# Performance work log

Hardware: AMD Instinct MI355X
Metric: run time of the kernel (lower is better)

## Reference

```python
import jax, jax.numpy as jnp
import numpy as np
import math

B, S, D = 16, 577, 768          # batch, seq (24*24 grid + 1 cls), in_dim=att_dim
H, HD = 12, 64                  # heads, head_dim
GRID = 24                       # height = width; S = GRID*GRID + rpe_skip
RATIO = 1.9
ALPHA, BETA, GAMMA = 1.0 * RATIO, 2.0 * RATIO, 8.0 * RATIO
BETA_INT = int(BETA)            # 3
NUM_BUCKETS = (2 * BETA_INT + 1) ** 2 + 1  # 49 product buckets + 1 extra for skip (cls) = 50


def _piecewise_index(d):
    # iRPE piecewise bucket index (numpy, static). d: integer offsets.
    d = d.astype(np.float64)
    ad = np.abs(d)
    log_part = ALPHA + np.log(np.maximum(ad, 1e-9) / ALPHA) / math.log(GAMMA / ALPHA) * (BETA - ALPHA)
    y_out = np.sign(d) * np.clip(np.round(log_part), None, BETA)
    idx = np.where(ad <= ALPHA, np.round(d), y_out)
    return np.trunc(idx).astype(np.int64)  # torch .to(int) truncates toward zero


def make_rp_bucket():
    # 2D 'product' method bucket ids with skip=1 (cls token -> extra bucket)
    ii, jj = np.meshgrid(np.arange(GRID), np.arange(GRID), indexing='ij')
    pos = np.stack([ii.ravel(), jj.ravel()], axis=-1)          # (L,2)
    diff = pos[:, None, :] - pos[None, :, :]                    # (L,L,2)
    Sb = 2 * BETA_INT + 1
    r = _piecewise_index(diff[..., 0]) + BETA_INT               # [0, 2*beta_int]
    c = _piecewise_index(diff[..., 1]) + BETA_INT
    pid = r * Sb + c                                            # [0, 48]
    L = GRID * GRID
    bucket = np.full((L + 1, L + 1), NUM_BUCKETS - 1, dtype=np.int32)
    bucket[1:, 1:] = pid
    return jnp.asarray(bucket)


def setup_inputs() -> dict:
    key = jax.random.key(0)
    k1, k2, k3 = jax.random.split(key, 3)
    x = jax.random.normal(k1, (B, S, D), dtype=jnp.float32)
    w_qkv = jax.random.normal(k2, (3 * D, D), dtype=jnp.float32) * 0.02   # torch Linear weight (out,in)
    rpe_table = jax.random.normal(k3, (HD, NUM_BUCKETS), dtype=jnp.float32) * 0.02  # shared-head contextual table
    rp_bucket = make_rp_bucket()                                # (S,S) int32
    return {"x": x, "w_qkv": w_qkv, "rpe_table": rpe_table, "rp_bucket": rp_bucket}


def reference(x, w_qkv, rpe_table, rp_bucket):
    qkv = x @ w_qkv.T                                           # (B,S,3D)
    q, k, v = jnp.split(qkv, 3, axis=-1)
    # Faithful to torch source: plain reshape (B,S,D)->(B,H,S,HD) (no transpose-split)
    scale = 1.0 / jnp.sqrt(jnp.asarray(HD, x.dtype))
    q = q.reshape(B, H, S, HD) * scale
    k = k.reshape(B, H, S, HD)
    v = v.reshape(B, H, S, HD)
    qk = jnp.einsum('bhid,bhjd->bhij', q, k)                    # (B,H,S,S)
    # contextual rpe_k: bias[b,h,i,j] = (q[b,h,i] . rpe_table[:, rp_bucket[i,j]])
    ctx = jnp.einsum('bhid,dc->bhic', q, rpe_table)             # (B,H,S,NUM_BUCKETS)
    idx = jnp.broadcast_to(rp_bucket[None, None].astype(jnp.int32), (B, H, S, S))
    bias = jnp.take_along_axis(ctx, idx, axis=-1)               # (B,H,S,S)
    att = jax.nn.softmax(qk + bias, axis=-1)
    out = jnp.einsum('bhij,bhjd->bhid', att, v)                 # (B,H,S,HD)
    y = out.transpose(0, 2, 1, 3).reshape(B, S, D)              # out_proj is Identity (out_dim==att_dim)
    return y
```

## Files before the change

### kernel.cpp

```cpp
#include <hip/hip_runtime.h>

constexpr int BN_  = 16;
constexpr int SN_  = 577;
constexpr int SP_  = 640;
constexpr int DN_  = 768;
constexpr int HN_  = 12;
constexpr int HD_  = 64;
constexpr int NB_  = 50;
constexpr int MR_  = BN_ * SN_;
constexpr int MRP_ = 73 * 128;
constexpr int NQ_  = 3 * DN_;
constexpr int BHS_ = BN_ * HN_ * SN_;
constexpr int SHD_ = SN_ * HD_;

typedef __attribute__((ext_vector_type(8))) short short8;
typedef __attribute__((ext_vector_type(4))) float f32x4;

__device__ __forceinline__ short f2bf(float f) {
  union { float f; unsigned u; } v; v.f = f;
  unsigned r = (v.u + 0x7fffu + ((v.u >> 16) & 1u)) >> 16;
  return (short)r;
}

__device__ __forceinline__ float ex2(float x) {
  float r; asm("v_exp_f32 %0, %1" : "=v"(r) : "v"(x)); return r;
}

__device__ __forceinline__ unsigned cvtpk(float a, float b) {
  unsigned r; asm("v_cvt_pk_bf16_f32 %0, %1, %2" : "=v"(r) : "v"(a), "v"(b));
  return r;
}

__device__ __forceinline__ float bf2f(unsigned short u) {
  union { unsigned u; float f; } v; v.u = ((unsigned)u) << 16; return v.f;
}

__launch_bounds__(256)
__global__ void cvt_k(const float* __restrict__ src, short* __restrict__ dst,
                      int n_src, int n_dst) {
  const int i = (blockIdx.x * 256 + threadIdx.x) * 8;
  if (i >= n_dst) return;
  union { short8 v; short u[8]; } pk;
  if (i < n_src) {
    const float4 a = *(const float4*)(src + i);
    const float4 b = *(const float4*)(src + i + 4);
    pk.u[0] = f2bf(a.x); pk.u[1] = f2bf(a.y); pk.u[2] = f2bf(a.z); pk.u[3] = f2bf(a.w);
    pk.u[4] = f2bf(b.x); pk.u[5] = f2bf(b.y); pk.u[6] = f2bf(b.z); pk.u[7] = f2bf(b.w);
  } else {
#pragma unroll
    for (int j = 0; j < 8; ++j) pk.u[j] = 0;
  }
  *(short8*)(dst + i) = pk.v;
}

__launch_bounds__(256)
__global__ void rpb8_k(const int* __restrict__ rpb, unsigned char* __restrict__ rpbu8) {
  const int tid = blockIdx.x * 256 + threadIdx.x;
  if (tid >= SN_ * 160) return;
  const int i = tid / 160, c4 = tid - i * 160;
  const int j = c4 * 4;
  uchar4 o;
  o.x = (j     < SN_) ? (unsigned char)rpb[i * SN_ + j    ] : 0;
  o.y = (j + 1 < SN_) ? (unsigned char)rpb[i * SN_ + j + 1] : 0;
  o.z = (j + 2 < SN_) ? (unsigned char)rpb[i * SN_ + j + 2] : 0;
  o.w = (j + 3 < SN_) ? (unsigned char)rpb[i * SN_ + j + 3] : 0;
  *(uchar4*)(rpbu8 + (size_t)i * 640 + j) = o;
}

__launch_bounds__(256)
__global__ void qkv_mfma_k(const short* __restrict__ xb, const short* __restrict__ wb,
                           short* __restrict__ Qbf, short* __restrict__ Ksw,
                           short* __restrict__ Vbf) {
  __shared__ short At[128 * 64];
  __shared__ short Bt[128 * 64];
  const int t = threadIdx.x;
  const int w = t >> 6, lane = t & 63, g = lane >> 4, ln = lane & 15;
  const int wm = w >> 1, wn = w & 1;
  const int m0 = blockIdx.y * 128, n0 = blockIdx.x * 128;

  const int sr = t >> 1, su = (t & 1) * 4;
  const short* ga = xb + (size_t)(m0 + sr) * DN_ + su * 8;
  const short* gb = wb + (size_t)(n0 + sr) * DN_ + su * 8;
  short* la = At + sr * 64;
  short* lb = Bt + sr * 64;
  const int swr = sr & 7;

  f32x4 acc[4][4];
#pragma unroll
  for (int mt = 0; mt < 4; ++mt)
#pragma unroll
    for (int nt = 0; nt < 4; ++nt) acc[mt][nt] = (f32x4){0.f, 0.f, 0.f, 0.f};

  short8 ra[4], rb[4];
#pragma unroll
  for (int u = 0; u < 4; ++u) {
    ra[u] = *(const short8*)(ga + u * 8);
    rb[u] = *(const short8*)(gb + u * 8);
  }

  for (int k0 = 0; k0 < DN_; k0 += 64) {
    __syncthreads();
#pragma unroll
    for (int u = 0; u < 4; ++u) {
      *(short8*)(la + (((su + u) ^ swr) * 8)) = ra[u];
      *(short8*)(lb + (((su + u) ^ swr) * 8)) = rb[u];
    }
    __syncthreads();
    if (k0 + 64 < DN_) {
#pragma unroll
      for (int u = 0; u < 4; ++u) {
        ra[u] = *(const short8*)(ga + k0 + 64 + u * 8);
        rb[u] = *(const short8*)(gb + k0 + 64 + u * 8);
      }
    }
#pragma unroll
    for (int kc = 0; kc < 2; ++kc) {
      short8 af[4], bf[4];
#pragma unroll
      for (int mt = 0; mt < 4; ++mt) {
        const int row = wm * 64 + mt * 16 + ln;
        const int u = (kc * 4 + g) ^ (row & 7);
        af[mt] = *(const short8*)&At[row * 64 + u * 8];
      }
#pragma unroll
      for (int nt = 0; nt < 4; ++nt) {
        const int row = wn * 64 + nt * 16 + ln;
        const int u = (kc * 4 + g) ^ (row & 7);
        bf[nt] = *(const short8*)&Bt[row * 64 + u * 8];
      }
#pragma unroll
      for (int mt = 0; mt < 4; ++mt)
#pragma unroll
        for (int nt = 0; nt < 4; ++nt)
          acc[mt][nt] = __builtin_amdgcn_mfma_f32_16x16x32_bf16(af[mt], bf[nt], acc[mt][nt], 0, 0, 0);
    }
  }

  const int nw0  = n0 + wn * 64;
  const int secg = nw0 / DN_;
  const int cbw  = nw0 - secg * DN_;
  const float QSC = 0.18033688011112042f;
#pragma unroll
  for (int mt = 0; mt < 4; ++mt) {
#pragma unroll
    for (int r = 0; r < 4; ++r) {
      const int gm = m0 + wm * 64 + mt * 16 + 4 * g + r;
      if (gm >= MR_) continue;
      const int bb = gm / SN_;
      const int ss = gm - bb * SN_;
      const int pb = ss * DN_ + cbw;
#pragma unroll
      for (int nt = 0; nt < 4; ++nt) {
        const int p   = pb + nt * 16 + ln;
        const int hh  = p / SHD_;
        const int rem = p - hh * SHD_;
        const int ii  = rem >> 6;
        const int dd  = rem & 63;
        const size_t ro = (size_t)(bb * HN_ + hh);
        const float v = acc[mt][nt][r];
        if (secg == 0) {
          Qbf[(ro * SN_ + ii) * 64 + dd] = f2bf(v * QSC);
        } else if (secg == 1) {
          Ksw[(ro * SP_ + ii) * 64 + (dd ^ ((ii & 7) << 3))] = f2bf(v);
        } else {
          Vbf[(ro * SP_ + ii) * 64 + dd] = f2bf(v);
        }
      }
    }
  }
}

__launch_bounds__(256)
__global__ void vtr_k(const short* __restrict__ Vbf, short* __restrict__ Vtsw) {
  __shared__ short T[64][72];
  const int t = threadIdx.x;
  const int jt = blockIdx.x, bh = blockIdx.y;
  const int j0 = jt * 64;
  {
    const int r = t >> 2, c0 = (t & 3) * 16;
    const short* src = Vbf + ((size_t)bh * SP_ + j0 + r) * 64 + c0;
    *(short8*)&T[r][c0]     = *(const short8*)(src);
    *(short8*)&T[r][c0 + 8] = *(const short8*)(src + 8);
  }
  __syncthreads();
  const int d = t >> 2;
  short* dst = Vtsw + ((size_t)bh * 64 + d) * SP_;
  const int sw = (d & 7) << 3;
#pragma unroll
  for (int e = 0; e < 4; ++e) {
    const int jl = (t & 3) * 16 + e * 4;
    const int jg = j0 + jl;
    short4 v;
    v.x = (jg + 0 < SN_) ? T[jl + 0][d] : (short)0;
    v.y = (jg + 1 < SN_) ? T[jl + 1][d] : (short)0;
    v.z = (jg + 2 < SN_) ? T[jl + 2][d] : (short)0;
    v.w = (jg + 3 < SN_) ? T[jl + 3][d] : (short)0;
    *(short4*)&dst[jg ^ sw] = v;
  }
}

__launch_bounds__(256)
__global__ void attn_k(const short* __restrict__ Qbf, const short* __restrict__ Ksw,
                       const short* __restrict__ Vtsw, const float* __restrict__ rpe,
                       const unsigned char* __restrict__ rpbu8, float* __restrict__ y) {
  __shared__ short Kt[2 * 4096];
  __shared__ short Vt[2 * 4096];
  __shared__ unsigned char rpbt[2 * 5120];
  __shared__ unsigned short ctxs[4][16][53];
  short (*Rp)[64] = (short (*)[64])rpbt;

  const int t = threadIdx.x;
  const int w = t >> 6, lane = t & 63, g = lane >> 4, ln = lane & 15;
  const int wg = blockIdx.x;
  const int xcd = wg & 7, idx = wg >> 3;
  const int qt = idx % 10;
  const int bh = (idx / 10) * 8 + xcd;
  const int b = bh / HN_, h = bh - b * HN_;
  const int i0 = qt * 64;
  const size_t rb = (size_t)bh * SN_;
  const short* Kbh = Ksw + (size_t)bh * SP_ * 64;
  const short* Vbh = Vtsw + (size_t)bh * 64 * SP_;

  const int tK = t * 8;
  const int vRow = t >> 3, vCol = (t & 7) * 8;
  const int rpRow = t >> 2, rpCol = (t & 3) * 16;
  const int irow_s = (i0 + rpRow <= SN_ - 1) ? (i0 + rpRow) : (SN_ - 1);

  short8 kr0, kr1, vr0, vr1; int4 rp_;
  kr0 = *(const short8*)(Kbh + tK);
  kr1 = *(const short8*)(Kbh + 2048 + tK);
  vr0 = *(const short8*)(Vbh + (size_t)vRow * SP_ + vCol);
  vr1 = *(const short8*)(Vbh + (size_t)(32 + vRow) * SP_ + vCol);
  rp_ = *(const int4*)(rpbu8 + (size_t)irow_s * 640 + rpCol);

  for (int e = t; e < 64 * 64; e += 256) {
    const int c = e >> 6, d = e & 63;
    Rp[c][d] = (c < NB_) ? f2bf(rpe[d * NB_ + c]) : (short)0;
  }

  short8 qf[2];
  {
    int row = i0 + 16 * w + ln; if (row > SN_ - 1) row = SN_ - 1;
    const short* qp = Qbf + (rb + row) * 64;
    qf[0] = *(const short8*)(qp + 8 * g);
    qf[1] = *(const short8*)(qp + 32 + 8 * g);
  }

  __syncthreads();

  {
    f32x4 accC[4];
#pragma unroll
    for (int ct = 0; ct < 4; ++ct) accC[ct] = (f32x4){0.f, 0.f, 0.f, 0.f};
#pragma unroll
    for (int kc = 0; kc < 2; ++kc) {
#pragma unroll
      for (int ct = 0; ct < 4; ++ct) {
        const short8 rf = *(const short8*)&Rp[ct * 16 + ln][kc * 32 + 8 * g];
        accC[ct] = __builtin_amdgcn_mfma_f32_16x16x32_bf16(qf[kc], rf, accC[ct], 0, 0, 0);
      }
    }
    __syncthreads();
#pragma unroll
    for (int ct = 0; ct < 4; ++ct) {
      const int c = ct * 16 + ln;
      if (c < 53) {
#pragma unroll
        for (int r = 0; r < 4; ++r)
          ctxs[w][4 * g + r][c] = (unsigned short)f2bf(accC[ct][r]);
      }
    }
  }

  *(short8*)&Kt[tK]        = kr0;
  *(short8*)&Kt[2048 + tK] = kr1;
  *(short8*)&Vt[tK]        = vr0;
  *(short8*)&Vt[2048 + tK] = vr1;
  *(int4*)&rpbt[rpRow * 80 + rpCol] = rp_;
  kr0 = *(const short8*)(Kbh + 4096 + tK);
  kr1 = *(const short8*)(Kbh + 4096 + 2048 + tK);
  vr0 = *(const short8*)(Vbh + (size_t)vRow * SP_ + 64 + vCol);
  vr1 = *(const short8*)(Vbh + (size_t)(32 + vRow) * SP_ + 64 + vCol);
  rp_ = *(const int4*)(rpbu8 + (size_t)irow_s * 640 + 64 + rpCol);
  __syncthreads();

  float m = -3e38f, l = 0.f;
  f32x4 accO[4];
#pragma unroll
  for (int dt = 0; dt < 4; ++dt) accO[dt] = (f32x4){0.f, 0.f, 0.f, 0.f};

  const int swv = (ln & 7) << 3;
  const unsigned short* cbase = &ctxs[w][ln][0];
  const int rpoff = (16 * w + ln) * 80;

  int cur = 0;
  for (int jt = 0; jt < 10; ++jt) {
    const int cw = cur ^ 1;
    if (jt < 9) {
      *(short8*)&Kt[cw * 4096 + tK]        = kr0;
      *(short8*)&Kt[cw * 4096 + 2048 + tK] = kr1;
      *(short8*)&Vt[cw * 4096 + tK]        = vr0;
      *(short8*)&Vt[cw * 4096 + 2048 + tK] = vr1;
      *(int4*)&rpbt[cw * 5120 + rpRow * 80 + rpCol] = rp_;
    }
    if (jt < 8) {
      const int jn = jt * 64 + 128;
      kr0 = *(const short8*)(Kbh + (size_t)jn * 64 + tK);
      kr1 = *(const short8*)(Kbh + (size_t)jn * 64 + 2048 + tK);
      vr0 = *(const short8*)(Vbh + (size_t)vRow * SP_ + jn + vCol);
      vr1 = *(const short8*)(Vbh + (size_t)(32 + vRow) * SP_ + jn + vCol);
      rp_ = *(const int4*)(rpbu8 + (size_t)irow_s * 640 + jn + rpCol);
    }

    const short* KtC = Kt + cur * 4096;
    const short* VtC = Vt + cur * 4096;
    const unsigned char* rpC = rpbt + cur * 5120;

    f32x4 accS[4];
#pragma unroll
    for (int nt = 0; nt < 4; ++nt) accS[nt] = (f32x4){0.f, 0.f, 0.f, 0.f};
    __builtin_amdgcn_s_setprio(1);
#pragma unroll
    for (int kc = 0; kc < 2; ++kc) {
      const int cb = (kc * 32 + 8 * g) ^ swv;
#pragma unroll
      for (int nt = 0; nt < 4; ++nt) {
        const short8 kf = *(const short8*)&KtC[(nt * 16 + ln) * 64 + cb];
        accS[nt] = __builtin_amdgcn_mfma_f32_16x16x32_bf16(kf, qf[kc], accS[nt], 0, 0, 0);
      }
    }
    __builtin_amdgcn_s_setprio(0);

    float pv[4][4];
#pragma unroll
    for (int nt = 0; nt < 4; ++nt) {
      const uchar4 bk = *(const uchar4*)&rpC[rpoff + nt * 16 + 4 * g];
      pv[nt][0] = accS[nt][0] + bf2f(cbase[bk.x]);
      pv[nt][1] = accS[nt][1] + bf2f(cbase[bk.y]);
      pv[nt][2] = accS[nt][2] + bf2f(cbase[bk.z]);
      pv[nt][3] = accS[nt][3] + bf2f(cbase[bk.w]);
    }
    if (jt == 9) {
#pragma unroll
      for (int nt = 0; nt < 4; ++nt) {
        const int jb = jt * 64 + nt * 16 + 4 * g;
#pragma unroll
        for (int r = 0; r < 4; ++r)
          if (jb + r >= SN_) pv[nt][r] = -3e38f;
      }
    }

    float mq[4];
#pragma unroll
    for (int nt = 0; nt < 4; ++nt)
      mq[nt] = fmaxf(fmaxf(pv[nt][0], pv[nt][1]), fmaxf(pv[nt][2], pv[nt][3]));
    float mx = fmaxf(fmaxf(mq[0], mq[1]), fmaxf(mq[2], mq[3]));
    mx = fmaxf(mx, __shfl_xor(mx, 16));
    mx = fmaxf(mx, __shfl_xor(mx, 32));

    if (__any(mx > m + 8.f)) {
      const float mnew = fmaxf(m, mx);
      const float sc = ex2(m - mnew);
      float scr[4];
#pragma unroll
      for (int r = 0; r < 4; ++r) scr[r] = __shfl(sc, 4 * g + r);
#pragma unroll
      for (int dt = 0; dt < 4; ++dt)
#pragma unroll
        for (int r = 0; r < 4; ++r) accO[dt][r] *= scr[r];
      l *= sc;
      m = mnew;
    }

#pragma unroll
    for (int nt = 0; nt < 4; ++nt)
#pragma unroll
      for (int r = 0; r < 4; ++r)
        pv[nt][r] = ex2(pv[nt][r] - m);
    float sq[4];
#pragma unroll
    for (int nt = 0; nt < 4; ++nt)
      sq[nt] = (pv[nt][0] + pv[nt][1]) + (pv[nt][2] + pv[nt][3]);
    float sum = (sq[0] + sq[1]) + (sq[2] + sq[3]);
    sum += __shfl_xor(sum, 16);
    sum += __shfl_xor(sum, 32);
    l += sum;

    short8 pf[2];
#pragma unroll
    for (int kc = 0; kc < 2; ++kc) {
      union { short8 v; unsigned wd[4]; } pk;
      pk.wd[0] = cvtpk(pv[2 * kc][0],     pv[2 * kc][1]);
      pk.wd[1] = cvtpk(pv[2 * kc][2],     pv[2 * kc][3]);
      pk.wd[2] = cvtpk(pv[2 * kc + 1][0], pv[2 * kc + 1][1]);
      pk.wd[3] = cvtpk(pv[2 * kc + 1][2], pv[2 * kc + 1][3]);
      pf[kc] = pk.v;
    }

    __builtin_amdgcn_s_setprio(1);
#pragma unroll
    for (int kc = 0; kc < 2; ++kc) {
#pragma unroll
      for (int dt = 0; dt < 4; ++dt) {
        const short* vrow = &VtC[(dt * 16 + ln) * 64];
        union { short8 v; short4 hh[2]; } u;
        u.hh[0] = *(const short4*)&vrow[(kc * 32 + 4 * g) ^ swv];
        u.hh[1] = *(const short4*)&vrow[(kc * 32 + 16 + 4 * g) ^ swv];
        accO[dt] = __builtin_amdgcn_mfma_f32_16x16x32_bf16(pf[kc], u.v, accO[dt], 0, 0, 0);
      }
    }
    __builtin_amdgcn_s_setprio(0);

    __syncthreads();
    cur ^= 1;
  }

  float linv[4];
#pragma unroll
  for (int r = 0; r < 4; ++r) linv[r] = 1.f / __shfl(l, 4 * g + r);
#pragma unroll
  for (int r = 0; r < 4; ++r) {
    const int i = i0 + 16 * w + 4 * g + r;
    if (i >= SN_) continue;
    float* yp = y + ((size_t)b * SN_ + i) * DN_ + h * HD_ + ln;
#pragma unroll
    for (int dt = 0; dt < 4; ++dt) yp[dt * 16] = accO[dt][r] * linv[r];
  }
}

extern "C" void kernel_launch(void* const* d_in, const int* in_sizes, int n_in,
                              void* d_out, int out_size, void* d_ws, size_t ws_size,
                              hipStream_t stream) {
  const float* x   = (const float*)d_in[0];
  const float* w   = (const float*)d_in[1];
  const float* rpe = (const float*)d_in[2];
  const int*   rpb = (const int*)d_in[3];
  float* y = (float*)d_out;

  short* xb   = (short*)d_ws;
  short* wb   = xb + (size_t)MRP_ * DN_;
  short* Qbf  = wb + (size_t)NQ_ * DN_;
  short* Ksw  = Qbf + (size_t)BHS_ * HD_;
  short* Vbf  = Ksw + (size_t)BN_ * HN_ * SP_ * 64;
  short* Vtsw = Vbf + (size_t)BN_ * HN_ * SP_ * 64;
  unsigned char* rpbu8 = (unsigned char*)(Vtsw + (size_t)BN_ * HN_ * 64 * SP_);

  cvt_k<<<dim3(MRP_ * DN_ / 2048), 256, 0, stream>>>(x, xb, MR_ * DN_, MRP_ * DN_);
  cvt_k<<<dim3(NQ_ * DN_ / 2048), 256, 0, stream>>>(w, wb, NQ_ * DN_, NQ_ * DN_);
  rpb8_k<<<dim3((SN_ * 160 + 255) / 256), 256, 0, stream>>>(rpb, rpbu8);
  qkv_mfma_k<<<dim3(18, 73), 256, 0, stream>>>(xb, wb, Qbf, Ksw, Vbf);
  vtr_k<<<dim3(10, BN_ * HN_), 256, 0, stream>>>(Vbf, Vtsw);
  attn_k<<<dim3(1920), 256, 0, stream>>>(Qbf, Ksw, Vtsw, rpe, rpbu8, y);
}
```

Before: 162.6 us.

## Process 128 query rows per block, reusing K/V tiles across two subtiles

Each wave now handles two 16-row query subtiles, so a block covers 128 query rows and half as many blocks are launched. Every K and V fragment read from shared memory feeds two MFMAs, which halves global and LDS traffic for K/V per query row. The LDS double buffer is replaced by a single buffer with register prefetch and two barriers per iteration. V transpose storage is permuted so PV operands load as one short8 instead of two short4. Register pressure rises, and the loss of LDS double-buffering plus the smaller grid may reduce overlap and occupancy.

```diff
diff --git a/kernel.cpp b/kernel.cpp
--- a/kernel.cpp
+++ b/kernel.cpp
@@ -195,7 +195,10 @@
     v.y = (jg + 1 < SN_) ? T[jl + 1][d] : (short)0;
     v.z = (jg + 2 < SN_) ? T[jl + 2][d] : (short)0;
     v.w = (jg + 3 < SN_) ? T[jl + 3][d] : (short)0;
-    *(short4*)&dst[jg ^ sw] = v;
+    const int oq = (jg >> 2) & 7;
+    const int pq = ((oq & 3) << 1) | (oq >> 2);
+    const int p  = (jg & ~31) | (pq << 2);
+    *(short4*)&dst[p ^ sw] = v;
   }
 }
 
@@ -203,228 +206,230 @@
 __global__ void attn_k(const short* __restrict__ Qbf, const short* __restrict__ Ksw,
                        const short* __restrict__ Vtsw, const float* __restrict__ rpe,
                        const unsigned char* __restrict__ rpbu8, float* __restrict__ y) {
-  __shared__ short Kt[2 * 4096];
-  __shared__ short Vt[2 * 4096];
-  __shared__ unsigned char rpbt[2 * 5120];
-  __shared__ unsigned short ctxs[4][16][53];
+  __shared__ short Kt[4096];
+  __shared__ short Vt[4096];
+  __shared__ unsigned char rpbt[128 * 68];
+  __shared__ unsigned short ctxs[4][32][53];
   short (*Rp)[64] = (short (*)[64])rpbt;
 
   const int t = threadIdx.x;
   const int w = t >> 6, lane = t & 63, g = lane >> 4, ln = lane & 15;
   const int wg = blockIdx.x;
   const int xcd = wg & 7, idx = wg >> 3;
-  const int qt = idx % 10;
-  const int bh = (idx / 10) * 8 + xcd;
+  const int qt = idx % 5;
+  const int bh = (idx / 5) * 8 + xcd;
   const int b = bh / HN_, h = bh - b * HN_;
-  const int i0 = qt * 64;
+  const int i0 = qt * 128;
   const size_t rb = (size_t)bh * SN_;
   const short* Kbh = Ksw + (size_t)bh * SP_ * 64;
   const short* Vbh = Vtsw + (size_t)bh * 64 * SP_;
 
   const int tK = t * 8;
   const int vRow = t >> 3, vCol = (t & 7) * 8;
-  const int rpRow = t >> 2, rpCol = (t & 3) * 16;
+  const int rpRow = t >> 1, rpCol = (t & 1) * 32;
   const int irow_s = (i0 + rpRow <= SN_ - 1) ? (i0 + rpRow) : (SN_ - 1);
 
-  short8 kr0, kr1, vr0, vr1; int4 rp_;
+  short8 kr0, kr1, vr0, vr1; int4 rp0_, rp1_;
   kr0 = *(const short8*)(Kbh + tK);
   kr1 = *(const short8*)(Kbh + 2048 + tK);
   vr0 = *(const short8*)(Vbh + (size_t)vRow * SP_ + vCol);
   vr1 = *(const short8*)(Vbh + (size_t)(32 + vRow) * SP_ + vCol);
-  rp_ = *(const int4*)(rpbu8 + (size_t)irow_s * 640 + rpCol);
+  rp0_ = *(const int4*)(rpbu8 + (size_t)irow_s * 640 + rpCol);
+  rp1_ = *(const int4*)(rpbu8 + (size_t)irow_s * 640 + rpCol + 16);
 
   for (int e = t; e < 64 * 64; e += 256) {
     const int c = e >> 6, d = e & 63;
     Rp[c][d] = (c < NB_) ? f2bf(rpe[d * NB_ + c]) : (short)0;
   }
 
-  short8 qf[2];
+  short8 qf[2][2];
+#pragma unroll
+  for (int s = 0; s < 2; ++s) {
+    int row = i0 + 32 * w + 16 * s + ln; if (row > SN_ - 1) row = SN_ - 1;
+    const short* qp = Qbf + (rb + row) * 64;
+    qf[s][0] = *(const short8*)(qp + 8 * g);
+    qf[s][1] = *(const short8*)(qp + 32 + 8 * g);
+  }
+
+  __syncthreads();
+
   {
-    int row = i0 + 16 * w + ln; if (row > SN_ - 1) row = SN_ - 1;
-    const short* qp = Qbf + (rb + row) * 64;
-    qf[0] = *(const short8*)(qp + 8 * g);
-    qf[1] = *(const short8*)(qp + 32 + 8 * g);
-  }
-
-  __syncthreads();
-
-  {
-    f32x4 accC[4];
-#pragma unroll
-    for (int ct = 0; ct < 4; ++ct) accC[ct] = (f32x4){0.f, 0.f, 0.f, 0.f};
+    f32x4 accC[2][4];
+#pragma unroll
+    for (int s = 0; s < 2; ++s)
+#pragma unroll
+      for (int ct = 0; ct < 4; ++ct) accC[s][ct] = (f32x4){0.f, 0.f, 0.f, 0.f};
 #pragma unroll
     for (int kc = 0; kc < 2; ++kc) {
 #pragma unroll
       for (int ct = 0; ct < 4; ++ct) {
         const short8 rf = *(const short8*)&Rp[ct * 16 + ln][kc * 32 + 8 * g];
-        accC[ct] = __builtin_amdgcn_mfma_f32_16x16x32_bf16(qf[kc], rf, accC[ct], 0, 0, 0);
-      }
-    }
+        accC[0][ct] = __builtin_amdgcn_mfma_f32_16x16x32_bf16(qf[0][kc], rf, accC[0][ct], 0, 0, 0);
+        accC[1][ct] = __builtin_amdgcn_mfma_f32_16x16x32_bf16(qf[1][kc], rf, accC[1][ct], 0, 0, 0);
+      }
+    }
+#pragma unroll
+    for (int s = 0; s < 2; ++s)
+#pragma unroll
+      for (int ct = 0; ct < 4; ++ct) {
+        const int c = ct * 16 + ln;
+        if (c < 53) {
+#pragma unroll
+          for (int r = 0; r < 4; ++r)
+            ctxs[w][16 * s + 4 * g + r][c] = (unsigned short)f2bf(accC[s][ct][r]);
+        }
+      }
+  }
+
+  float m0s = -3e38f, m1s = -3e38f, l0s = 0.f, l1s = 0.f;
+  f32x4 accO[2][4];
+#pragma unroll
+  for (int s = 0; s < 2; ++s)
+#pragma unroll
+    for (int dt = 0; dt < 4; ++dt) accO[s][dt] = (f32x4){0.f, 0.f, 0.f, 0.f};
+
+  const int swv = (ln & 7) << 3;
+
+  for (int jt = 0; jt < 10; ++jt) {
     __syncthreads();
-#pragma unroll
-    for (int ct = 0; ct < 4; ++ct) {
-      const int c = ct * 16 + ln;
-      if (c < 53) {
-#pragma unroll
-        for (int r = 0; r < 4; ++r)
-          ctxs[w][4 * g + r][c] = (unsigned short)f2bf(accC[ct][r]);
-      }
-    }
-  }
-
-  *(short8*)&Kt[tK]        = kr0;
-  *(short8*)&Kt[2048 + tK] = kr1;
-  *(short8*)&Vt[tK]        = vr0;
-  *(short8*)&Vt[2048 + tK] = vr1;
-  *(int4*)&rpbt[rpRow * 80 + rpCol] = rp_;
-  kr0 = *(const short8*)(Kbh + 4096 + tK);
-  kr1 = *(const short8*)(Kbh + 4096 + 2048 + tK);
-  vr0 = *(const short8*)(Vbh + (size_t)vRow * SP_ + 64 + vCol);
-  vr1 = *(const short8*)(Vbh + (size_t)(32 + vRow) * SP_ + 64 + vCol);
-  rp_ = *(const int4*)(rpbu8 + (size_t)irow_s * 640 + 64 + rpCol);
-  __syncthreads();
-
-  float m = -3e38f, l = 0.f;
-  f32x4 accO[4];
-#pragma unroll
-  for (int dt = 0; dt < 4; ++dt) accO[dt] = (f32x4){0.f, 0.f, 0.f, 0.f};
-
-  const int swv = (ln & 7) << 3;
-  const unsigned short* cbase = &ctxs[w][ln][0];
-  const int rpoff = (16 * w + ln) * 80;
-
-  int cur = 0;
-  for (int jt = 0; jt < 10; ++jt) {
-    const int cw = cur ^ 1;
+    *(short8*)&Kt[tK]        = kr0;
+    *(short8*)&Kt[2048 + tK] = kr1;
+    *(short8*)&Vt[tK]        = vr0;
+    *(short8*)&Vt[2048 + tK] = vr1;
+    *(int4*)&rpbt[rpRow * 68 + rpCol]      = rp0_;
+    *(int4*)&rpbt[rpRow * 68 + rpCol + 16] = rp1_;
+    __syncthreads();
+
     if (jt < 9) {
-      *(short8*)&Kt[cw * 4096 + tK]        = kr0;
-      *(short8*)&Kt[cw * 4096 + 2048 + tK] = kr1;
-      *(short8*)&Vt[cw * 4096 + tK]        = vr0;
-      *(short8*)&Vt[cw * 4096 + 2048 + tK] = vr1;
-      *(int4*)&rpbt[cw * 5120 + rpRow * 80 + rpCol] = rp_;
-    }
-    if (jt < 8) {
-      const int jn = jt * 64 + 128;
+      const int jn = jt * 64 + 64;
       kr0 = *(const short8*)(Kbh + (size_t)jn * 64 + tK);
       kr1 = *(const short8*)(Kbh + (size_t)jn * 64 + 2048 + tK);
       vr0 = *(const short8*)(Vbh + (size_t)vRow * SP_ + jn + vCol);
       vr1 = *(const short8*)(Vbh + (size_t)(32 + vRow) * SP_ + jn + vCol);
-      rp_ = *(const int4*)(rpbu8 + (size_t)irow_s * 640 + jn + rpCol);
-    }
-
-    const short* KtC = Kt + cur * 4096;
-    const short* VtC = Vt + cur * 4096;
-    const unsigned char* rpC = rpbt + cur * 5120;
-
-    f32x4 accS[4];
-#pragma unroll
-    for (int nt = 0; nt < 4; ++nt) accS[nt] = (f32x4){0.f, 0.f, 0.f, 0.f};
+      rp0_ = *(const int4*)(rpbu8 + (size_t)irow_s * 640 + jn + rpCol);
+      rp1_ = *(const int4*)(rpbu8 + (size_t)irow_s * 640 + jn + rpCol + 16);
+    }
+
+    f32x4 accS[2][4];
+#pragma unroll
+    for (int s = 0; s < 2; ++s)
+#pragma unroll
+      for (int nt = 0; nt < 4; ++nt) accS[s][nt] = (f32x4){0.f, 0.f, 0.f, 0.f};
     __builtin_amdgcn_s_setprio(1);
 #pragma unroll
     for (int kc = 0; kc < 2; ++kc) {
       const int cb = (kc * 32 + 8 * g) ^ swv;
 #pragma unroll
       for (int nt = 0; nt < 4; ++nt) {
-        const short8 kf = *(const short8*)&KtC[(nt * 16 + ln) * 64 + cb];
-        accS[nt] = __builtin_amdgcn_mfma_f32_16x16x32_bf16(kf, qf[kc], accS[nt], 0, 0, 0);
+        const short8 kf = *(const short8*)&Kt[(nt * 16 + ln) * 64 + cb];
+        accS[0][nt] = __builtin_amdgcn_mfma_f32_16x16x32_bf16(kf, qf[0][kc], accS[0][nt], 0, 0, 0);
+        accS[1][nt] = __builtin_amdgcn_mfma_f32_16x16x32_bf16(kf, qf[1][kc], accS[1][nt], 0, 0, 0);
       }
     }
     __builtin_amdgcn_s_setprio(0);
 
-    float pv[4][4];
-#pragma unroll
-    for (int nt = 0; nt < 4; ++nt) {
-      const uchar4 bk = *(const uchar4*)&rpC[rpoff + nt * 16 + 4 * g];
-      pv[nt][0] = accS[nt][0] + bf2f(cbase[bk.x]);
-      pv[nt][1] = accS[nt][1] + bf2f(cbase[bk.y]);
-      pv[nt][2] = accS[nt][2] + bf2f(cbase[bk.z]);
-      pv[nt][3] = accS[nt][3] + bf2f(cbase[bk.w]);
-    }
-    if (jt == 9) {
+    short8 pf[2][2];
+#pragma unroll
+    for (int s = 0; s < 2; ++s) {
+      const unsigned short* cbase = &ctxs[w][16 * s + ln][0];
+      const int rpoff = (32 * w + 16 * s + ln) * 68;
+      float pv[4][4];
 #pragma unroll
       for (int nt = 0; nt < 4; ++nt) {
-        const int jb = jt * 64 + nt * 16 + 4 * g;
+        const uchar4 bk = *(const uchar4*)&rpbt[rpoff + nt * 16 + 4 * g];
+        pv[nt][0] = accS[s][nt][0] + bf2f(cbase[bk.x]);
+        pv[nt][1] = accS[s][nt][1] + bf2f(cbase[bk.y]);
+        pv[nt][2] = accS[s][nt][2] + bf2f(cbase[bk.z]);
+        pv[nt][3] = accS[s][nt][3] + bf2f(cbase[bk.w]);
+      }
+      if (jt == 9) {
+#pragma unroll
+        for (int nt = 0; nt < 4; ++nt) {
+          const int jb = jt * 64 + nt * 16 + 4 * g;
+#pragma unroll
+          for (int r = 0; r < 4; ++r)
+            if (jb + r >= SN_) pv[nt][r] = -3e38f;
+        }
+      }
+
+      float& m = (s == 0) ? m0s : m1s;
+      float& l = (s == 0) ? l0s : l1s;
+
+      float mq[4];
+#pragma unroll
+      for (int nt = 0; nt < 4; ++nt)
+        mq[nt] = fmaxf(fmaxf(pv[nt][0], pv[nt][1]), fmaxf(pv[nt][2], pv[nt][3]));
+      float mx = fmaxf(fmaxf(mq[0], mq[1]), fmaxf(mq[2], mq[3]));
+      mx = fmaxf(mx, __shfl_xor(mx, 16));
+      mx = fmaxf(mx, __shfl_xor(mx, 32));
+
+      if (__any(mx > m + 8.f)) {
+        const float mnew = fmaxf(m, mx);
+        const float sc = ex2(m - mnew);
+        float scr[4];
+#pragma unroll
+        for (int r = 0; r < 4; ++r) scr[r] = __shfl(sc, 4 * g + r);
+#pragma unroll
+        for (int dt = 0; dt < 4; ++dt)
+#pragma unroll
+          for (int r = 0; r < 4; ++r) accO[s][dt][r] *= scr[r];
+        l *= sc;
+        m = mnew;
+      }
+
+#pragma unroll
+      for (int nt = 0; nt < 4; ++nt)
 #pragma unroll
         for (int r = 0; r < 4; ++r)
-          if (jb + r >= SN_) pv[nt][r] = -3e38f;
-      }
-    }
-
-    float mq[4];
-#pragma unroll
-    for (int nt = 0; nt < 4; ++nt)
-      mq[nt] = fmaxf(fmaxf(pv[nt][0], pv[nt][1]), fmaxf(pv[nt][2], pv[nt][3]));
-    float mx = fmaxf(fmaxf(mq[0], mq[1]), fmaxf(mq[2], mq[3]));
-    mx = fmaxf(mx, __shfl_xor(mx, 16));
-    mx = fmaxf(mx, __shfl_xor(mx, 32));
-
-    if (__any(mx > m + 8.f)) {
-      const float mnew = fmaxf(m, mx);
-      const float sc = ex2(m - mnew);
-      float scr[4];
-#pragma unroll
-      for (int r = 0; r < 4; ++r) scr[r] = __shfl(sc, 4 * g + r);
-#pragma unroll
-      for (int dt = 0; dt < 4; ++dt)
-#pragma unroll
-        for (int r = 0; r < 4; ++r) accO[dt][r] *= scr[r];
-      l *= sc;
-      m = mnew;
-    }
-
-#pragma unroll
-    for (int nt = 0; nt < 4; ++nt)
-#pragma unroll
-      for (int r = 0; r < 4; ++r)
-        pv[nt][r] = ex2(pv[nt][r] - m);
-    float sq[4];
-#pragma unroll
-    for (int nt = 0; nt < 4; ++nt)
-      sq[nt] = (pv[nt][0] + pv[nt][1]) + (pv[nt][2] + pv[nt][3]);
-    float sum = (sq[0] + sq[1]) + (sq[2] + sq[3]);
-    sum += __shfl_xor(sum, 16);
-    sum += __shfl_xor(sum, 32);
-    l += sum;
-
-    short8 pf[2];
+          pv[nt][r] = ex2(pv[nt][r] - m);
+      float sq[4];
+#pragma unroll
+      for (int nt = 0; nt < 4; ++nt)
+        sq[nt] = (pv[nt][0] + pv[nt][1]) + (pv[nt][2] + pv[nt][3]);
+      float sum = (sq[0] + sq[1]) + (sq[2] + sq[3]);
+      sum += __shfl_xor(sum, 16);
+      sum += __shfl_xor(sum, 32);
+      l += sum;
+
+#pragma unroll
+      for (int kc = 0; kc < 2; ++kc) {
+        union { short8 v; unsigned wd[4]; } pk;
+        pk.wd[0] = cvtpk(pv[2 * kc][0],     pv[2 * kc][1]);
+        pk.wd[1] = cvtpk(pv[2 * kc][2],     pv[2 * kc][3]);
+        pk.wd[2] = cvtpk(pv[2 * kc + 1][0], pv[2 * kc + 1][1]);
+        pk.wd[3] = cvtpk(pv[2 * kc + 1][2], pv[2 * kc + 1][3]);
+        pf[s][kc] = pk.v;
+      }
+    }
+
+    __builtin_amdgcn_s_setprio(1);
 #pragma unroll
     for (int kc = 0; kc < 2; ++kc) {
-      union { short8 v; unsigned wd[4]; } pk;
-      pk.wd[0] = cvtpk(pv[2 * kc][0],     pv[2 * kc][1]);
-      pk.wd[1] = cvtpk(pv[2 * kc][2],     pv[2 * kc][3]);
-      pk.wd[2] = cvtpk(pv[2 * kc + 1][0], pv[2 * kc + 1][1]);
-      pk.wd[3] = cvtpk(pv[2 * kc + 1][2], pv[2 * kc + 1][3]);
-      pf[kc] = pk.v;
-    }
-
-    __builtin_amdgcn_s_setprio(1);
-#pragma unroll
-    for (int kc = 0; kc < 2; ++kc) {
+      const int cb = (kc * 32 + 8 * g) ^ swv;
 #pragma unroll
       for (int dt = 0; dt < 4; ++dt) {
-        const short* vrow = &VtC[(dt * 16 + ln) * 64];
-        union { short8 v; short4 hh[2]; } u;
-        u.hh[0] = *(const short4*)&vrow[(kc * 32 + 4 * g) ^ swv];
-        u.hh[1] = *(const short4*)&vrow[(kc * 32 + 16 + 4 * g) ^ swv];
-        accO[dt] = __builtin_amdgcn_mfma_f32_16x16x32_bf16(pf[kc], u.v, accO[dt], 0, 0, 0);
+        const short8 vf = *(const short8*)&Vt[(dt * 16 + ln) * 64 + cb];
+        accO[0][dt] = __builtin_amdgcn_mfma_f32_16x16x32_bf16(pf[0][kc], vf, accO[0][dt], 0, 0, 0);
+        accO[1][dt] = __builtin_amdgcn_mfma_f32_16x16x32_bf16(pf[1][kc], vf, accO[1][dt], 0, 0, 0);
       }
     }
     __builtin_amdgcn_s_setprio(0);
-
-    __syncthreads();
-    cur ^= 1;
-  }
-
-  float linv[4];
-#pragma unroll
-  for (int r = 0; r < 4; ++r) linv[r] = 1.f / __shfl(l, 4 * g + r);
-#pragma unroll
-  for (int r = 0; r < 4; ++r) {
-    const int i = i0 + 16 * w + 4 * g + r;
-    if (i >= SN_) continue;
-    float* yp = y + ((size_t)b * SN_ + i) * DN_ + h * HD_ + ln;
-#pragma unroll
-    for (int dt = 0; dt < 4; ++dt) yp[dt * 16] = accO[dt][r] * linv[r];
+  }
+
+#pragma unroll
+  for (int s = 0; s < 2; ++s) {
+    const float lv = (s == 0) ? l0s : l1s;
+    float linv[4];
+#pragma unroll
+    for (int r = 0; r < 4; ++r) linv[r] = 1.f / __shfl(lv, 4 * g + r);
+#pragma unroll
+    for (int r = 0; r < 4; ++r) {
+      const int i = i0 + 32 * w + 16 * s + 4 * g + r;
+      if (i >= SN_) continue;
+      float* yp = y + ((size_t)b * SN_ + i) * DN_ + h * HD_ + ln;
+#pragma unroll
+      for (int dt = 0; dt < 4; ++dt) yp[dt * 16] = accO[s][dt][r] * linv[r];
+    }
   }
 }
 
@@ -450,5 +455,5 @@
   rpb8_k<<<dim3((SN_ * 160 + 255) / 256), 256, 0, stream>>>(rpb, rpbu8);
   qkv_mfma_k<<<dim3(18, 73), 256, 0, stream>>>(xb, wb, Qbf, Ksw, Vbf);
   vtr_k<<<dim3(10, BN_ * HN_), 256, 0, stream>>>(Vbf, Vtsw);
-  attn_k<<<dim3(1920), 256, 0, stream>>>(Qbf, Ksw, Vtsw, rpe, rpbu8, y);
-}
+  attn_k<<<dim3(960), 256, 0, stream>>>(Qbf, Ksw, Vtsw, rpe, rpbu8, y);
+}
```

New measurement: 149.9 us. 1.08x faster.
